# Kernel tuning notes

Measured on AMD Instinct MI355X. Metric: run time of the kernel, lower is better.

Reference implementation:

```python
import jax, jax.numpy as jnp
import numpy as np

B, S, HID, NH, HD, RD = 1, 2048, 2560, 32, 80, 64
SCALE = HD ** -0.5
NEG = -1e9


def _alibi_slopes(n):
    # n = 32 is a power of two -> standard geometric slopes 2^(-8i/n)
    return jnp.asarray(2.0 ** (-8.0 * np.arange(1, n + 1) / n), dtype=jnp.float32)


def _rope(x, pos):
    # GPT-NeoX style rotary on the first RD dims of each head; x: [B,S,NH,HD]
    inv_freq = 1.0 / (10000.0 ** (np.arange(0, RD, 2, dtype=np.float32) / RD))  # [RD/2]
    ang = pos.astype(jnp.float32)[..., None] * jnp.asarray(inv_freq)  # [B,S,RD/2]
    cos = jnp.cos(ang)[:, :, None, :]  # [B,S,1,RD/2]
    sin = jnp.sin(ang)[:, :, None, :]
    x1 = x[..., : RD // 2]
    x2 = x[..., RD // 2 : RD]
    rot = jnp.concatenate([x1 * cos - x2 * sin, x2 * cos + x1 * sin], axis=-1)
    return jnp.concatenate([rot, x[..., RD:]], axis=-1)


def setup_inputs() -> dict:
    key = jax.random.key(0)
    k1, k2, k3 = jax.random.split(key, 3)
    return {
        "position_ids": jnp.arange(B * S, dtype=jnp.int32).reshape(B, S) % S,
        "hidden_states": jax.random.normal(k1, (B, S, HID), dtype=jnp.float32),
        "w_qkv": jax.random.normal(k2, (HID, 3 * HID), dtype=jnp.float32) * 0.02,
        "w_out": jax.random.normal(k3, (HID, HID), dtype=jnp.float32) * 0.02,
    }


def reference(position_ids, hidden_states, w_qkv, w_out):
    qkv = hidden_states @ w_qkv                       # [B,S,3*HID]
    q, k, v = jnp.split(qkv, 3, axis=-1)
    q = _rope(q.reshape(B, S, NH, HD), position_ids)
    k = _rope(k.reshape(B, S, NH, HD), position_ids)
    v = v.reshape(B, S, NH, HD)

    scores = jnp.einsum("bqhd,bkhd->bhqk", q, k) * SCALE  # [B,NH,S,S]
    rel = (position_ids[:, None, :] - position_ids[:, :, None]).astype(jnp.float32)  # j - i
    slopes = _alibi_slopes(NH)
    bias = slopes[None, :, None, None] * rel[:, None, :, :]  # [B,NH,S,S]
    causal = rel <= 0.0
    scores = jnp.where(causal[:, None, :, :], scores + bias, NEG)
    attn = jax.nn.softmax(scores, axis=-1)
    out = jnp.einsum("bhqk,bkhd->bqhd", attn, v).reshape(B, S, HID)
    return out @ w_out
```

## Files before the change

### kernel.cpp

```cpp
#include <hip/hip_runtime.h>
#include <type_traits>
#include <utility>

typedef unsigned short u16;
typedef unsigned int u32;
typedef __attribute__((ext_vector_type(8))) short short8;
typedef __attribute__((ext_vector_type(8))) __bf16 bhalf8;
typedef __attribute__((ext_vector_type(4))) short short4v;
typedef __attribute__((ext_vector_type(4))) __bf16 bhalf4;
typedef __attribute__((ext_vector_type(4))) float f32x4;
typedef __attribute__((ext_vector_type(4))) unsigned short us4;

#define S_LEN 2048
#define NHEAD 32
#define HD 80
#define HDP 96
#define HID 2560
#define N3 7680
#define QK_SCALE 0.11180339887498949f
#define LOG2E 1.4426950408889634f

template <typename T, typename = void> struct MfmaTakes : std::false_type {};
template <typename T>
struct MfmaTakes<T, std::void_t<decltype(__builtin_amdgcn_mfma_f32_16x16x32_bf16(
                       std::declval<T>(), std::declval<T>(), std::declval<f32x4>(), 0, 0, 0))>>
    : std::true_type {};

template <typename AB>
__device__ inline f32x4 mfma_raw(AB a, AB b, f32x4 c) {
  return __builtin_amdgcn_mfma_f32_16x16x32_bf16(a, b, c, 0, 0, 0);
}
using mfma_ab_t = std::conditional_t<MfmaTakes<bhalf8>::value, bhalf8, short8>;
__device__ inline f32x4 MFMA(short8 a, short8 b, f32x4 c) {
  return mfma_raw<mfma_ab_t>(__builtin_bit_cast(mfma_ab_t, a),
                             __builtin_bit_cast(mfma_ab_t, b), c);
}

#if defined(__has_builtin)
#if __has_builtin(__builtin_amdgcn_mfma_f32_16x16x16bf16_1k)
#define MFMA16_RAW(a, b, c) __builtin_amdgcn_mfma_f32_16x16x16bf16_1k(a, b, c, 0, 0, 0)
#define HAVE_MFMA16 1
#elif __has_builtin(__builtin_amdgcn_mfma_f32_16x16x16_bf16)
#define MFMA16_RAW(a, b, c) __builtin_amdgcn_mfma_f32_16x16x16_bf16(a, b, c, 0, 0, 0)
#define HAVE_MFMA16 1
#endif
#endif

#ifdef HAVE_MFMA16
template <typename T, typename = void> struct M16Takes : std::false_type {};
template <typename T>
struct M16Takes<T, std::void_t<decltype(MFMA16_RAW(std::declval<T>(), std::declval<T>(),
                                                   std::declval<f32x4>()))>> : std::true_type {};
using m16_t = std::conditional_t<M16Takes<bhalf4>::value, bhalf4, short4v>;
__device__ inline f32x4 MFMA16(short4v a, short4v b, f32x4 c) {
  return MFMA16_RAW(__builtin_bit_cast(m16_t, a), __builtin_bit_cast(m16_t, b), c);
}
#else
__device__ inline f32x4 MFMA16(short4v a, short4v b, f32x4 c) {
  short8 a8 = {a[0], a[1], a[2], a[3], 0, 0, 0, 0};
  short8 b8 = {b[0], b[1], b[2], b[3], 0, 0, 0, 0};
  return MFMA(a8, b8, c);
}
#endif

__device__ inline float bf2f(u16 b) { return __uint_as_float(((u32)b) << 16); }
__device__ inline u16 f2bf(float f) {
  u32 u = __float_as_uint(f);
  u += 0x7fffu + ((u >> 16) & 1u);
  return (u16)(u >> 16);
}

typedef __attribute__((address_space(1))) void as1_void;
typedef __attribute__((address_space(3))) void as3_void;

#if defined(__has_builtin)
#if __has_builtin(__builtin_amdgcn_global_load_lds)
#define HAVE_GLL 1
#endif
#endif

__device__ inline void stage16(const u16* g, u16* lds_base, int lane) {
#ifdef HAVE_GLL
  (void)lane;
  __builtin_amdgcn_global_load_lds((as1_void*)g, (as3_void*)lds_base, 16, 0, 0);
#else
  *(short8*)(lds_base + lane * 8) = *(const short8*)g;
#endif
}

__device__ inline void sched_barrier0() {
#if defined(__has_builtin)
#if __has_builtin(__builtin_amdgcn_sched_barrier)
  __builtin_amdgcn_sched_barrier(0);
#endif
#endif
}

__global__ __launch_bounds__(256) void detect_dtype(const u32* __restrict__ words,
                                                    int* __restrict__ flag) {
  __shared__ int red[256];
  int junk = 0;
  for (int i = threadIdx.x; i < 2048; i += 256) {
    u16 lo = (u16)(words[i] & 0xffffu);
    u32 e = (lo >> 7) & 0xffu;
    junk += (e >= 137u);
  }
  red[threadIdx.x] = junk;
  __syncthreads();
  for (int s = 128; s > 0; s >>= 1) {
    if (threadIdx.x < s) red[threadIdx.x] += red[threadIdx.x + s];
    __syncthreads();
  }
  if (threadIdx.x == 0) flag[0] = (red[0] > 64) ? 1 : 0;
}

__global__ __launch_bounds__(256) void convert_hidden(const void* __restrict__ in,
                                                      u16* __restrict__ out, int n4,
                                                      const int* __restrict__ flagp) {
  const int f = *flagp;
  int i = blockIdx.x * 256 + threadIdx.x;
  if (i >= n4) return;
  if (f) {
    const float* inf = (const float*)in;
    us4 o;
#pragma unroll
    for (int j = 0; j < 4; ++j) o[j] = f2bf(inf[(size_t)i * 4 + j]);
    *(us4*)&out[(size_t)i * 4] = o;
  } else {
    *(us4*)&out[(size_t)i * 4] = *(const us4*)&((const u16*)in)[(size_t)i * 4];
  }
}

__global__ __launch_bounds__(256) void transpose64(const void* __restrict__ in,
                                                   u16* __restrict__ out,
                                                   int istride, int ioff, int ostride,
                                                   const int* __restrict__ flagp) {
  __shared__ u16 tile[64][66];
  const int f = flagp ? *flagp : 0;
  const int bx = blockIdx.x * 64, by = blockIdx.y * 64;
  const int tx4 = (threadIdx.x & 15) * 4, ty = threadIdx.x >> 4;
#pragma unroll
  for (int i = 0; i < 4; ++i) {
    const int row = ty + i * 16;
    const size_t idx = (size_t)(by + row) * istride + ioff + bx + tx4;
    us4 v;
    if (f) {
      const f32x4 x = *(const f32x4*)&((const float*)in)[idx];
#pragma unroll
      for (int j = 0; j < 4; ++j) v[j] = f2bf(x[j]);
    } else {
      v = *(const us4*)&((const u16*)in)[idx];
    }
    *(u32*)&tile[row][tx4] = (u32)v[0] | ((u32)v[1] << 16);
    *(u32*)&tile[row][tx4 + 2] = (u32)v[2] | ((u32)v[3] << 16);
  }
  __syncthreads();
#pragma unroll
  for (int i = 0; i < 4; ++i) {
    const int oc = ty + i * 16;
    us4 o;
#pragma unroll
    for (int j = 0; j < 4; ++j) o[j] = tile[tx4 + j][oc];
    *(us4*)&out[(size_t)(bx + oc) * ostride + by + tx4] = o;
  }
}

__global__ __launch_bounds__(256, 2) void gemm128c(const u16* __restrict__ A,
                                                   const u16* __restrict__ Bt,
                                                   void* __restrict__ C,
                                                   int M, int N, int K,
                                                   const int* __restrict__ flagp) {
  __shared__ u16 As[2][128 * 64];
  __shared__ u16 Bs[2][128 * 64];
  const int tid = threadIdx.x;
  const int w = tid >> 6, l = tid & 63, la = l & 15, qd = l >> 4;
  const int wr = w >> 1, wc = w & 1;
  const int of32 = flagp ? *flagp : 0;

  const int nbx = gridDim.x;
  const int nwg = nbx * gridDim.y;
  int lin = blockIdx.y * nbx + blockIdx.x;
  if ((nwg & 7) == 0) lin = (lin & 7) * (nwg >> 3) + (lin >> 3);
  const int m0 = (lin / nbx) * 128, n0 = (lin % nbx) * 128;
  const int NT = K >> 6;

  const int sx0 = (qd ^ (la & 7)) * 8;
  const int sx1 = ((4 + qd) ^ (la & 7)) * 8;
  const int gsw = ((tid & 7) ^ ((tid >> 3) & 7)) * 8;

  f32x4 acc[4][4] = {};

  auto issue = [&](int s) {
    if (s >= NT * 4) return;
    const int kt = s >> 2, part = s & 3, buf = kt & 1;
    const int h = part & 1;
    const u16* G = (part >= 2) ? A : Bt;
    const int b0 = (part >= 2) ? m0 : n0;
    u16* L = ((part >= 2) ? &As[buf][0] : &Bs[buf][0]) + h * 4096;
    const int k0 = kt << 6;
#pragma unroll
    for (int q = 0; q < 2; ++q) {
      const int row = h * 64 + q * 32 + (tid >> 3);
      const u16* g = G + (size_t)(b0 + row) * K + k0 + gsw;
      stage16(g, L + (q * 256 + w * 64) * 8, l);
    }
  };

  auto readA = [&](int buf, int mh, short8(&af)[2][2]) {
    const u16* base = &As[buf][0];
#pragma unroll
    for (int i = 0; i < 2; ++i) {
      const int ro = (wr * 64 + mh * 32 + i * 16 + la) * 64;
      af[i][0] = *(const short8*)(base + ro + sx0);
      af[i][1] = *(const short8*)(base + ro + sx1);
    }
  };
  auto readB = [&](int buf, int nh, short8(&bf)[2][2]) {
    const u16* base = &Bs[buf][0];
#pragma unroll
    for (int j = 0; j < 2; ++j) {
      const int ro = (wc * 64 + nh * 32 + j * 16 + la) * 64;
      bf[j][0] = *(const short8*)(base + ro + sx0);
      bf[j][1] = *(const short8*)(base + ro + sx1);
    }
  };
  auto quad = [&](short8(&af)[2][2], short8(&bf)[2][2], int mh, int nh) {
#pragma unroll
    for (int kk = 0; kk < 2; ++kk)
#pragma unroll
      for (int i = 0; i < 2; ++i)
#pragma unroll
        for (int jj = 0; jj < 2; ++jj)
          acc[mh * 2 + i][nh * 2 + jj] =
              MFMA(af[i][kk], bf[jj][kk], acc[mh * 2 + i][nh * 2 + jj]);
  };

#pragma unroll
  for (int s = 0; s < 6; ++s) issue(s);
  asm volatile("s_waitcnt vmcnt(4)" ::: "memory");
  __builtin_amdgcn_s_barrier();

  for (int t = 0; t < NT; ++t) {
    const int buf = t & 1;
    short8 af[2][2], af2[2][2], bf0[2][2], bf1[2][2];
    readA(buf, 0, af);
    sched_barrier0();
    readB(buf, 0, bf0);
    sched_barrier0();
    readB(buf, 1, bf1);
    sched_barrier0();
    issue(4 * t + 6);
    issue(4 * t + 7);
    asm volatile("s_waitcnt lgkmcnt(4)" ::: "memory");
    sched_barrier0();
    readA(buf, 1, af2);
    sched_barrier0();
    __builtin_amdgcn_s_setprio(1);
    quad(af, bf0, 0, 0);
    __builtin_amdgcn_s_setprio(0);
    asm volatile("s_waitcnt lgkmcnt(4)" ::: "memory");
    sched_barrier0();
    __builtin_amdgcn_s_setprio(1);
    quad(af, bf1, 0, 1);
    __builtin_amdgcn_s_setprio(0);
    __builtin_amdgcn_s_barrier();
    issue(4 * t + 8);
    issue(4 * t + 9);
    asm volatile("s_waitcnt lgkmcnt(0)" ::: "memory");
    sched_barrier0();
    __builtin_amdgcn_s_setprio(1);
    quad(af2, bf0, 1, 0);
    quad(af2, bf1, 1, 1);
    __builtin_amdgcn_s_setprio(0);
    asm volatile("s_waitcnt vmcnt(4)" ::: "memory");
    __builtin_amdgcn_s_barrier();
  }

#pragma unroll
  for (int i = 0; i < 4; ++i)
#pragma unroll
    for (int j = 0; j < 4; ++j) {
      const int r0 = m0 + wr * 64 + (i >> 1) * 32 + (i & 1) * 16 + qd * 4;
      const int c0 = n0 + wc * 64 + (j >> 1) * 32 + (j & 1) * 16 + la;
#pragma unroll
      for (int r = 0; r < 4; ++r) {
        if (of32)
          ((float*)C)[(size_t)(r0 + r) * N + c0] = acc[i][j][r];
        else
          ((u16*)C)[(size_t)(r0 + r) * N + c0] = f2bf(acc[i][j][r]);
      }
    }
}

__global__ __launch_bounds__(512, 2) void gemm256(const u16* __restrict__ A,
                                                  const u16* __restrict__ Bt,
                                                  u16* __restrict__ C,
                                                  int M, int N, int K) {
  __shared__ u16 As[2][256 * 64];
  __shared__ u16 Bs[2][256 * 64];
  const int tid = threadIdx.x;
  const int w = tid >> 6, l = tid & 63, la = l & 15, qd = l >> 4;
  const int wr = w >> 2, wc = w & 3;

  const int nbx = gridDim.x;
  const int nwg = nbx * gridDim.y;
  int lin = blockIdx.y * nbx + blockIdx.x;
  if ((nwg & 7) == 0) lin = (lin & 7) * (nwg >> 3) + (lin >> 3);
  const int m0 = (lin / nbx) * 256, n0 = (lin % nbx) * 256;
  const int NT = K >> 6;

  const int sx0 = (qd ^ (la & 7)) * 8;
  const int sx1 = ((4 + qd) ^ (la & 7)) * 8;
  const int gsw = ((tid & 7) ^ ((tid >> 3) & 7)) * 8;

  f32x4 acc[8][4] = {};

  auto issue = [&](int s) {
    if (s >= NT * 4) return;
    const int kt = s >> 2, part = s & 3, buf = kt & 1;
    const int h = part & 1;
    const u16* G = (part >= 2) ? A : Bt;
    const int b0 = (part >= 2) ? m0 : n0;
    u16* L = ((part >= 2) ? &As[buf][0] : &Bs[buf][0]) + h * 8192;
    const int k0 = kt << 6;
#pragma unroll
    for (int q = 0; q < 2; ++q) {
      const int row = h * 128 + q * 64 + (tid >> 3);
      const u16* g = G + (size_t)(b0 + row) * K + k0 + gsw;
      stage16(g, L + (q * 512 + w * 64) * 8, l);
    }
  };

  auto readA = [&](int buf, int mh, short8(&af)[4][2]) {
    const u16* base = &As[buf][0];
#pragma unroll
    for (int i = 0; i < 4; ++i) {
      const int ro = (wr * 128 + mh * 64 + i * 16 + la) * 64;
      af[i][0] = *(const short8*)(base + ro + sx0);
      af[i][1] = *(const short8*)(base + ro + sx1);
    }
  };
  auto readB = [&](int buf, int nh, short8(&bf)[2][2]) {
    const u16* base = &Bs[buf][0];
#pragma unroll
    for (int j = 0; j < 2; ++j) {
      const int ro = (wc * 64 + nh * 32 + j * 16 + la) * 64;
      bf[j][0] = *(const short8*)(base + ro + sx0);
      bf[j][1] = *(const short8*)(base + ro + sx1);
    }
  };
  auto quad = [&](short8(&af)[4][2], short8(&bf)[2][2], int mh, int nh) {
#pragma unroll
    for (int kk = 0; kk < 2; ++kk)
#pragma unroll
      for (int i = 0; i < 4; ++i)
#pragma unroll
        for (int jj = 0; jj < 2; ++jj)
          acc[mh * 4 + i][nh * 2 + jj] =
              MFMA(af[i][kk], bf[jj][kk], acc[mh * 4 + i][nh * 2 + jj]);
  };

#pragma unroll
  for (int s = 0; s < 6; ++s) issue(s);
  asm volatile("s_waitcnt vmcnt(4)" ::: "memory");
  __builtin_amdgcn_s_barrier();

  for (int t = 0; t < NT; ++t) {
    const int buf = t & 1;
    short8 af[4][2], af2[4][2], bf0[2][2], bf1[2][2];
    readA(buf, 0, af);
    sched_barrier0();
    readB(buf, 0, bf0);
    sched_barrier0();
    readB(buf, 1, bf1);
    sched_barrier0();
    issue(4 * t + 6);
    issue(4 * t + 7);
    asm volatile("s_waitcnt lgkmcnt(4)" ::: "memory");
    sched_barrier0();
    readA(buf, 1, af2);
    sched_barrier0();
    __builtin_amdgcn_s_setprio(1);
    quad(af, bf0, 0, 0);
    __builtin_amdgcn_s_setprio(0);
    asm volatile("s_waitcnt lgkmcnt(8)" ::: "memory");
    sched_barrier0();
    __builtin_amdgcn_s_setprio(1);
    quad(af, bf1, 0, 1);
    __builtin_amdgcn_s_setprio(0);
    __builtin_amdgcn_s_barrier();
    issue(4 * t + 8);
    issue(4 * t + 9);
    asm volatile("s_waitcnt lgkmcnt(0)" ::: "memory");
    sched_barrier0();
    __builtin_amdgcn_s_setprio(1);
    quad(af2, bf0, 1, 0);
    quad(af2, bf1, 1, 1);
    __builtin_amdgcn_s_setprio(0);
    asm volatile("s_waitcnt vmcnt(4)" ::: "memory");
    __builtin_amdgcn_s_barrier();
  }

#pragma unroll
  for (int i = 0; i < 8; ++i)
#pragma unroll
    for (int j = 0; j < 4; ++j) {
      const int r0 = m0 + wr * 128 + i * 16 + qd * 4;
      const int c0 = n0 + wc * 64 + j * 16 + la;
#pragma unroll
      for (int r = 0; r < 4; ++r)
        C[(size_t)(r0 + r) * N + c0] = f2bf(acc[i][j][r]);
    }
}

__global__ __launch_bounds__(256) void rope_prep(const u16* __restrict__ qkv,
                                                 const int* __restrict__ pos,
                                                 u16* __restrict__ Qh,
                                                 u16* __restrict__ Kt) {
  const int s = blockIdx.x;
  const int h = blockIdx.y * 4 + (threadIdx.x >> 6);
  const int t = threadIdx.x & 63;
  const size_t qin = (size_t)s * N3 + h * HD;
  const size_t kin = qin + HID;
  const size_t ob = ((size_t)h * S_LEN + s) * HDP;
  const size_t kb = ((size_t)(h * 32) + (s >> 6)) * 6144 + (size_t)(s & 63) * 8;
  if (t < 32) {
    const float p = (float)pos[s];
    const float inv = exp2f(-(float)t * (13.287712379549449f / 32.0f));
    const float ang = p * inv;
    const float cs = cosf(ang), sn = sinf(ang);
    float x1 = bf2f(qkv[qin + t]), x2 = bf2f(qkv[qin + t + 32]);
    Qh[ob + t] = f2bf(x1 * cs - x2 * sn);
    Qh[ob + t + 32] = f2bf(x2 * cs + x1 * sn);
    x1 = bf2f(qkv[kin + t]);
    x2 = bf2f(qkv[kin + t + 32]);
    Kt[kb + (size_t)(t >> 3) * 512 + (t & 7)] = f2bf(x1 * cs - x2 * sn);
    const int d2 = t + 32;
    Kt[kb + (size_t)(d2 >> 3) * 512 + (d2 & 7)] = f2bf(x2 * cs + x1 * sn);
  } else if (t < 48) {
    const int d = t + 32;
    Qh[ob + d] = qkv[qin + d];
    Kt[kb + (size_t)(d >> 3) * 512 + (d & 7)] = qkv[kin + d];
  } else {
    const int d = t + 32;
    Qh[ob + d] = 0;
    Kt[kb + (size_t)(d >> 3) * 512 + (d & 7)] = 0;
  }
}

__global__ __launch_bounds__(512, 4) void attn_fused(const u16* __restrict__ Qh,
                                                     const u16* __restrict__ Kt,
                                                     const u16* __restrict__ Vt,
                                                     u16* __restrict__ AO) {
  __shared__ u16 Ks[2][768 * 8];
  __shared__ u16 Vs[2][640 * 8];
  const int tid = threadIdx.x, w = tid >> 6, l = tid & 63;
  const int la = l & 15, qd = l >> 4;
  const int h = blockIdx.y;
  const int p = blockIdx.x;
  const int tile = (h < 16) ? p : 15 - p;
  const int q0 = tile * 128;
  const int nIt = 2 * tile + 2;
  const size_t hS = (size_t)h * S_LEN;

  const int qb = q0 + w * 16;
  const int q = qb + la;
  short8 qf[3];
#pragma unroll
  for (int c = 0; c < 3; ++c)
    qf[c] = *(const short8*)&Qh[(hS + qb + la) * HDP + c * 32 + qd * 8];

  const float slope2 = exp2f(-0.25f * (float)(h + 1)) * LOG2E;
  const float scl2 = QK_SCALE * LOG2E;
  float m_i = -1e30f, l_i = 0.f;
  f32x4 acc[5] = {};

  const u16* gK = Kt + (size_t)h * 32 * 6144;
  const u16* gV = Vt + (size_t)h * HD * S_LEN;

  auto stage = [&](int kt_g, int buf) {
    const u16* gkt = gK + (size_t)kt_g * 6144;
    stage16(gkt + (size_t)(w * 64 + l) * 8, &Ks[buf][(w * 64) * 8], l);
    if (w < 4)
      stage16(gkt + (size_t)(512 + w * 64 + l) * 8, &Ks[buf][(512 + w * 64) * 8], l);
    const u16* gv = gV + (kt_g << 6);
    {
      const int c = w * 64 + l;
      const int row = c >> 3, seg = c & 7;
      const int gcol = ((seg - (row & 7)) & 7) * 8;
      stage16(gv + (size_t)row * S_LEN + gcol, &Vs[buf][(w * 64) * 8], l);
    }
    if (w < 2) {
      const int c = 512 + w * 64 + l;
      const int row = c >> 3, seg = c & 7;
      const int gcol = ((seg - (row & 7)) & 7) * 8;
      stage16(gv + (size_t)row * S_LEN + gcol, &Vs[buf][(512 + w * 64) * 8], l);
    }
  };

  stage(0, 0);
  for (int it = 0; it < nIt; ++it) {
    const int buf = it & 1;
    __syncthreads();
    if (it + 1 < nIt) stage(it + 1, buf ^ 1);
    const int k0 = it << 6;
    if (k0 >= qb + 16) continue;

    f32x4 st[4];
#pragma unroll
    for (int kt = 0; kt < 4; ++kt) {
      short8 kf[3];
#pragma unroll
      for (int c = 0; c < 3; ++c)
        kf[c] = *(const short8*)&Ks[buf][((c * 4 + qd) * 64 + kt * 16 + la) * 8];
      f32x4 z = {};
#pragma unroll
      for (int c = 0; c < 3; ++c) z = MFMA(kf[c], qf[c], z);
      st[kt] = z;
    }

    const float base = (float)(k0 + qd * 4 - q);
    float mloc = -1e30f;
    if (k0 + 64 <= qb + 1) {
#pragma unroll
      for (int kt = 0; kt < 4; ++kt)
#pragma unroll
        for (int r = 0; r < 4; ++r) {
          const float rel = base + (float)(kt * 16 + r);
          const float v = st[kt][r] * scl2 + slope2 * rel;
          st[kt][r] = v;
          mloc = fmaxf(mloc, v);
        }
    } else {
#pragma unroll
      for (int kt = 0; kt < 4; ++kt)
#pragma unroll
        for (int r = 0; r < 4; ++r) {
          const float rel = base + (float)(kt * 16 + r);
          const float v = (rel <= 0.f) ? st[kt][r] * scl2 + slope2 * rel : -1e30f;
          st[kt][r] = v;
          mloc = fmaxf(mloc, v);
        }
    }
    mloc = fmaxf(mloc, __shfl_xor(mloc, 16));
    mloc = fmaxf(mloc, __shfl_xor(mloc, 32));

    if (!__all(mloc - m_i <= 8.0f)) {
      const float nm = fmaxf(m_i, mloc);
      const float al = exp2f(m_i - nm);
      m_i = nm;
      l_i *= al;
#pragma unroll
      for (int dt = 0; dt < 5; ++dt) acc[dt] *= al;
    }

    float ps = 0.f;
    short4v pf[4];
#pragma unroll
    for (int kt = 0; kt < 4; ++kt) {
      short4v pk;
#pragma unroll
      for (int r = 0; r < 4; ++r) {
        const float pv = exp2f(st[kt][r] - m_i);
        ps += pv;
        pk[r] = (short)f2bf(pv);
      }
      pf[kt] = pk;
    }
    ps += __shfl_xor(ps, 16);
    ps += __shfl_xor(ps, 32);
    l_i += ps;

    const int cb = qd * 4 + ((la & 7) << 3);
#pragma unroll
    for (int dt = 0; dt < 5; ++dt) {
      const int vrow = (dt * 16 + la) * 64;
#pragma unroll
      for (int kt = 0; kt < 4; ++kt) {
        const short4v vf = *(const short4v*)&Vs[buf][vrow + ((kt * 16 + cb) & 63)];
        acc[dt] = MFMA16(vf, pf[kt], acc[dt]);
      }
    }
  }

  const float inv = 1.0f / l_i;
  const size_t row = (size_t)q;
#pragma unroll
  for (int dt = 0; dt < 5; ++dt) {
    us4 o;
#pragma unroll
    for (int r = 0; r < 4; ++r) o[r] = f2bf(acc[dt][r] * inv);
    *(us4*)&AO[row * HID + h * HD + dt * 16 + qd * 4] = o;
  }
}

extern "C" void kernel_launch(void* const* d_in, const int* in_sizes, int n_in,
                              void* d_out, int out_size, void* d_ws, size_t ws_size,
                              hipStream_t stream) {
  const int* pos = (const int*)d_in[0];
  const void* hidden = d_in[1];
  const void* w_qkv = d_in[2];
  const void* w_out = d_in[3];
  u16* ws = (u16*)d_ws;

  u16* Hb = ws;
  u16* WtQ = Hb + (size_t)S_LEN * HID;
  u16* WtO = WtQ + (size_t)N3 * HID;
  u16* qkv = WtO + (size_t)HID * HID;
  int* flag = (int*)(qkv + (size_t)S_LEN * N3);
  u16* Vt = Hb;
  u16* Qh = WtQ;
  u16* Kh = Qh + (size_t)NHEAD * S_LEN * HDP;
  u16* AO = Kh + (size_t)NHEAD * S_LEN * HDP;

  detect_dtype<<<1, 256, 0, stream>>>((const u32*)hidden, flag);
  convert_hidden<<<(S_LEN * HID / 4 + 255) / 256, 256, 0, stream>>>(hidden, Hb,
                                                                    S_LEN * HID / 4, flag);
  transpose64<<<dim3(N3 / 64, HID / 64), 256, 0, stream>>>(w_qkv, WtQ, N3, 0, HID, flag);
  transpose64<<<dim3(HID / 64, HID / 64), 256, 0, stream>>>(w_out, WtO, HID, 0, HID, flag);
  gemm256<<<dim3(N3 / 256, S_LEN / 256), 512, 0, stream>>>(Hb, WtQ, qkv, S_LEN, N3, HID);
  transpose64<<<dim3(HID / 64, S_LEN / 64), 256, 0, stream>>>(qkv, Vt, N3, 2 * HID, S_LEN,
                                                              nullptr);
  rope_prep<<<dim3(S_LEN, NHEAD / 4), 256, 0, stream>>>(qkv, pos, Qh, Kh);
  attn_fused<<<dim3(16, NHEAD), 512, 0, stream>>>(Qh, Kh, Vt, AO);
  gemm128c<<<dim3(HID / 128, S_LEN / 128), 256, 0, stream>>>(AO, WtO, d_out, S_LEN, HID,
                                                             HID, flag);
}
```

Measured before the change: 389.4 us.

## Triple-buffer B tiles in GEMMs and drop mid-iteration barrier

The B operand's shared-memory staging goes from two buffers to three in both GEMM kernels. B loads for tile t+2 are now issued early in iteration t, alongside the A loads for t+1, instead of after a mid-loop barrier, and that barrier is removed. The aim is a deeper prefetch and one fewer workgroup sync per K-step. The cost is more LDS per workgroup. For gemm256 this reaches about 160KB, which likely allows only one workgroup per CU despite the launch bounds asking for two.

```diff
diff --git a/kernel.cpp b/kernel.cpp
--- a/kernel.cpp
+++ b/kernel.cpp
@@ -171,7 +171,7 @@
                                                    int M, int N, int K,
                                                    const int* __restrict__ flagp) {
   __shared__ u16 As[2][128 * 64];
-  __shared__ u16 Bs[2][128 * 64];
+  __shared__ u16 Bs[3][128 * 64];
   const int tid = threadIdx.x;
   const int w = tid >> 6, l = tid & 63, la = l & 15, qd = l >> 4;
   const int wr = w >> 1, wc = w & 1;
@@ -192,11 +192,11 @@
 
   auto issue = [&](int s) {
     if (s >= NT * 4) return;
-    const int kt = s >> 2, part = s & 3, buf = kt & 1;
+    const int kt = s >> 2, part = s & 3;
     const int h = part & 1;
     const u16* G = (part >= 2) ? A : Bt;
     const int b0 = (part >= 2) ? m0 : n0;
-    u16* L = ((part >= 2) ? &As[buf][0] : &Bs[buf][0]) + h * 4096;
+    u16* L = ((part >= 2) ? &As[kt & 1][0] : &Bs[kt % 3][0]) + h * 4096;
     const int k0 = kt << 6;
 #pragma unroll
     for (int q = 0; q < 2; ++q) {
@@ -241,19 +241,21 @@
   __builtin_amdgcn_s_barrier();
 
   for (int t = 0; t < NT; ++t) {
-    const int buf = t & 1;
+    const int ab = t & 1, bb = t % 3;
     short8 af[2][2], af2[2][2], bf0[2][2], bf1[2][2];
-    readA(buf, 0, af);
-    sched_barrier0();
-    readB(buf, 0, bf0);
-    sched_barrier0();
-    readB(buf, 1, bf1);
+    readA(ab, 0, af);
+    sched_barrier0();
+    readB(bb, 0, bf0);
+    sched_barrier0();
+    readB(bb, 1, bf1);
     sched_barrier0();
     issue(4 * t + 6);
     issue(4 * t + 7);
+    issue(4 * t + 8);
+    issue(4 * t + 9);
     asm volatile("s_waitcnt lgkmcnt(4)" ::: "memory");
     sched_barrier0();
-    readA(buf, 1, af2);
+    readA(ab, 1, af2);
     sched_barrier0();
     __builtin_amdgcn_s_setprio(1);
     quad(af, bf0, 0, 0);
@@ -263,9 +265,6 @@
     __builtin_amdgcn_s_setprio(1);
     quad(af, bf1, 0, 1);
     __builtin_amdgcn_s_setprio(0);
-    __builtin_amdgcn_s_barrier();
-    issue(4 * t + 8);
-    issue(4 * t + 9);
     asm volatile("s_waitcnt lgkmcnt(0)" ::: "memory");
     sched_barrier0();
     __builtin_amdgcn_s_setprio(1);
@@ -297,7 +296,7 @@
                                                   u16* __restrict__ C,
                                                   int M, int N, int K) {
   __shared__ u16 As[2][256 * 64];
-  __shared__ u16 Bs[2][256 * 64];
+  __shared__ u16 Bs[3][256 * 64];
   const int tid = threadIdx.x;
   const int w = tid >> 6, l = tid & 63, la = l & 15, qd = l >> 4;
   const int wr = w >> 2, wc = w & 3;
@@ -317,11 +316,11 @@
 
   auto issue = [&](int s) {
     if (s >= NT * 4) return;
-    const int kt = s >> 2, part = s & 3, buf = kt & 1;
+    const int kt = s >> 2, part = s & 3;
     const int h = part & 1;
     const u16* G = (part >= 2) ? A : Bt;
     const int b0 = (part >= 2) ? m0 : n0;
-    u16* L = ((part >= 2) ? &As[buf][0] : &Bs[buf][0]) + h * 8192;
+    u16* L = ((part >= 2) ? &As[kt & 1][0] : &Bs[kt % 3][0]) + h * 8192;
     const int k0 = kt << 6;
 #pragma unroll
     for (int q = 0; q < 2; ++q) {
@@ -366,19 +365,21 @@
   __builtin_amdgcn_s_barrier();
 
   for (int t = 0; t < NT; ++t) {
-    const int buf = t & 1;
+    const int ab = t & 1, bb = t % 3;
     short8 af[4][2], af2[4][2], bf0[2][2], bf1[2][2];
-    readA(buf, 0, af);
-    sched_barrier0();
-    readB(buf, 0, bf0);
-    sched_barrier0();
-    readB(buf, 1, bf1);
+    readA(ab, 0, af);
+    sched_barrier0();
+    readB(bb, 0, bf0);
+    sched_barrier0();
+    readB(bb, 1, bf1);
     sched_barrier0();
     issue(4 * t + 6);
     issue(4 * t + 7);
+    issue(4 * t + 8);
+    issue(4 * t + 9);
     asm volatile("s_waitcnt lgkmcnt(4)" ::: "memory");
     sched_barrier0();
-    readA(buf, 1, af2);
+    readA(ab, 1, af2);
     sched_barrier0();
     __builtin_amdgcn_s_setprio(1);
     quad(af, bf0, 0, 0);
@@ -388,9 +389,6 @@
     __builtin_amdgcn_s_setprio(1);
     quad(af, bf1, 0, 1);
     __builtin_amdgcn_s_setprio(0);
-    __builtin_amdgcn_s_barrier();
-    issue(4 * t + 8);
-    issue(4 * t + 9);
     asm volatile("s_waitcnt lgkmcnt(0)" ::: "memory");
     sched_barrier0();
     __builtin_amdgcn_s_setprio(1);
```

After: 372.8 us. 4.3% less time.
